# Kernel optimization log

Measured on AMD Instinct MI355X. Metric: run time of the kernel, lower is better.

## Reference

```python
import jax, jax.numpy as jnp
import numpy as np

B, N, H = 128, 512, 512
NEG_INF = -1e30


def setup_inputs() -> dict:
    key = jax.random.key(0)
    k1, k2, k3, k4 = jax.random.split(key, 4)
    code_feat = jax.random.normal(k1, (B, N, H), dtype=jnp.float32)
    node_mask = jax.random.randint(k2, (B, N), 0, 2, dtype=jnp.int32)
    node_mask = node_mask.at[:, 0].set(1)  # ensure >=1 valid node per sample
    scale = 1.0 / np.sqrt(H)
    W_sa = jax.random.normal(k3, (H, H), dtype=jnp.float32) * scale
    b_sa = jnp.zeros((H,), dtype=jnp.float32)
    w_sc = jax.random.normal(k4, (H,), dtype=jnp.float32) * scale
    b_sc = jnp.zeros((), dtype=jnp.float32)
    return {"code_feat": code_feat, "node_mask": node_mask,
            "W_sa": W_sa, "b_sa": b_sa, "w_sc": w_sc, "b_sc": b_sc}


def reference(code_feat, node_mask, W_sa, b_sa, w_sc, b_sc):
    # code_sa_tanh = self_atten_scalar(tanh(self_atten(code_feat)))  -> [B, N]
    h = jnp.tanh(jnp.einsum('bnh,hk->bnk', code_feat, W_sa) + b_sa)
    scores = jnp.einsum('bnk,k->bn', h, w_sc) + b_sc  # [B, N]
    valid = node_mask.astype(bool)
    # masked_select + softmax over selected nodes == masked softmax; invalid
    # positions get weight 0, so the weighted sum over all nodes matches the
    # original per-sample bmm over the ragged selection exactly.
    scores = jnp.where(valid, scores, NEG_INF)
    attn = jax.nn.softmax(scores, axis=1)  # [B, N]
    pooled = jnp.einsum('bn,bnh->bh', attn, code_feat)  # [B, H]
    return jnp.tanh(pooled)
```

## Files before the change

### kernel.cpp

```cpp
#include <hip/hip_runtime.h>

#define NEG_INF (-1e30f)

typedef __bf16 bf16x8 __attribute__((ext_vector_type(8)));
typedef float  f32x4  __attribute__((ext_vector_type(4)));
typedef unsigned short ushort;

__device__ __forceinline__ float fast_tanhf(float x) {
    return 1.0f - 2.0f / (1.0f + __expf(2.0f * x));
}

__device__ __forceinline__ ushort f2bf(float f) {
    union { float f; unsigned u; } v; v.f = f;
    unsigned r = v.u + 0x7fffu + ((v.u >> 16) & 1u);
    return (ushort)(r >> 16);
}

__device__ __forceinline__ void gload_lds16(const void* gsrc, void* ldsdst) {
    __builtin_amdgcn_global_load_lds(
        (const __attribute__((address_space(1))) unsigned int*)gsrc,
        (__attribute__((address_space(3))) unsigned int*)ldsdst, 16, 0, 0);
}

__global__ void convw_kernel(const float* __restrict__ W, ushort* __restrict__ Wt) {
    int i = blockIdx.x * 256 + threadIdx.x;
    int h = i >> 9, c = i & 511;
    Wt[c * 512 + h] = f2bf(W[i]);
}

__global__ __launch_bounds__(256) void gemm_scores_kernel(
    const float* __restrict__ feat, const ushort* __restrict__ Wt,
    const float* __restrict__ b_sa, const float* __restrict__ w_sc,
    float* __restrict__ sp) {

    __shared__ ushort Alds[2][4096];
    __shared__ ushort Blds[2][4096];
    __shared__ float  redE[4][64];

    const int tid  = threadIdx.x;
    const int id   = blockIdx.x;
    const int g    = id & 7;
    const int c8   = id >> 3;
    const int my   = g * 64 + (c8 >> 2);
    const int by   = c8 & 3;
    const int m0   = my * 128;
    const int n0   = by * 128;

    const int lane = tid & 63;
    const int wv   = tid >> 6;
    const int wm   = wv >> 1, wn = wv & 1;
    const int lr   = lane & 15;
    const int kg   = lane >> 4;

    const int arow = tid >> 1;
    const int aseg = (tid & 1) * 16;
    const float* agp = feat + (size_t)(m0 + arow) * 512 + aseg;
    const int wA = (arow >> 4) * 512 + (aseg >> 3) * 128 + (arow & 15) * 8;

    const ushort* bg0 = Wt + (size_t)(n0 + (0 * 4 + wv) * 16 + lr) * 512 + kg * 8;
    const ushort* bg1 = Wt + (size_t)(n0 + (1 * 4 + wv) * 16 + lr) * 512 + kg * 8;

    const int aBase = wm * 2048 + kg * 128 + lr * 8;
    const int bBase = wn * 2048 + kg * 128 + lr * 8;

    f32x4 acc[4][4];
#pragma unroll
    for (int a = 0; a < 4; ++a)
#pragma unroll
        for (int b = 0; b < 4; ++b) acc[a][b] = (f32x4){0.f, 0.f, 0.f, 0.f};

    float4 p0 = *reinterpret_cast<const float4*>(agp + 0);
    float4 p1 = *reinterpret_cast<const float4*>(agp + 4);
    float4 p2 = *reinterpret_cast<const float4*>(agp + 8);
    float4 p3 = *reinterpret_cast<const float4*>(agp + 12);
    gload_lds16(bg0, (char*)Blds[0] + wv * 1024);
    gload_lds16(bg1, (char*)Blds[0] + 4096 + wv * 1024);
    {
        bf16x8 h0, h1;
        h0[0] = (__bf16)p0.x; h0[1] = (__bf16)p0.y; h0[2] = (__bf16)p0.z; h0[3] = (__bf16)p0.w;
        h0[4] = (__bf16)p1.x; h0[5] = (__bf16)p1.y; h0[6] = (__bf16)p1.z; h0[7] = (__bf16)p1.w;
        h1[0] = (__bf16)p2.x; h1[1] = (__bf16)p2.y; h1[2] = (__bf16)p2.z; h1[3] = (__bf16)p2.w;
        h1[4] = (__bf16)p3.x; h1[5] = (__bf16)p3.y; h1[6] = (__bf16)p3.z; h1[7] = (__bf16)p3.w;
        *reinterpret_cast<bf16x8*>(&Alds[0][wA])       = h0;
        *reinterpret_cast<bf16x8*>(&Alds[0][wA + 128]) = h1;
    }
    p0 = *reinterpret_cast<const float4*>(agp + 32);
    p1 = *reinterpret_cast<const float4*>(agp + 36);
    p2 = *reinterpret_cast<const float4*>(agp + 40);
    p3 = *reinterpret_cast<const float4*>(agp + 44);
    __syncthreads();

    int p = 0;
    for (int k0 = 0; k0 < 512; k0 += 32) {
        if (k0 < 480) {
            bf16x8 h0, h1;
            h0[0] = (__bf16)p0.x; h0[1] = (__bf16)p0.y; h0[2] = (__bf16)p0.z; h0[3] = (__bf16)p0.w;
            h0[4] = (__bf16)p1.x; h0[5] = (__bf16)p1.y; h0[6] = (__bf16)p1.z; h0[7] = (__bf16)p1.w;
            h1[0] = (__bf16)p2.x; h1[1] = (__bf16)p2.y; h1[2] = (__bf16)p2.z; h1[3] = (__bf16)p2.w;
            h1[4] = (__bf16)p3.x; h1[5] = (__bf16)p3.y; h1[6] = (__bf16)p3.z; h1[7] = (__bf16)p3.w;
            *reinterpret_cast<bf16x8*>(&Alds[p ^ 1][wA])       = h0;
            *reinterpret_cast<bf16x8*>(&Alds[p ^ 1][wA + 128]) = h1;
            gload_lds16(bg0 + k0 + 32, (char*)Blds[p ^ 1] + wv * 1024);
            gload_lds16(bg1 + k0 + 32, (char*)Blds[p ^ 1] + 4096 + wv * 1024);
            if (k0 < 448) {
                p0 = *reinterpret_cast<const float4*>(agp + k0 + 64);
                p1 = *reinterpret_cast<const float4*>(agp + k0 + 68);
                p2 = *reinterpret_cast<const float4*>(agp + k0 + 72);
                p3 = *reinterpret_cast<const float4*>(agp + k0 + 76);
            }
        }
        bf16x8 af[4], bfv[4];
#pragma unroll
        for (int a = 0; a < 4; ++a)
            af[a] = *reinterpret_cast<const bf16x8*>(&Alds[p][aBase + a * 512]);
#pragma unroll
        for (int b = 0; b < 4; ++b)
            bfv[b] = *reinterpret_cast<const bf16x8*>(&Blds[p][bBase + b * 512]);
#pragma unroll
        for (int a = 0; a < 4; ++a)
#pragma unroll
            for (int b = 0; b < 4; ++b)
                acc[a][b] = __builtin_amdgcn_mfma_f32_16x16x32_bf16(
                    af[a], bfv[b], acc[a][b], 0, 0, 0);
        __syncthreads();
        p ^= 1;
    }

    float rsum[4][4];
#pragma unroll
    for (int a = 0; a < 4; ++a)
#pragma unroll
        for (int r = 0; r < 4; ++r) rsum[a][r] = 0.0f;

#pragma unroll
    for (int b = 0; b < 4; ++b) {
        int col = n0 + wn * 64 + b * 16 + lr;
        float wsc = w_sc[col];
        float bsa = b_sa[col];
#pragma unroll
        for (int a = 0; a < 4; ++a)
#pragma unroll
            for (int r = 0; r < 4; ++r)
                rsum[a][r] += fast_tanhf(acc[a][b][r] + bsa) * wsc;
    }
#pragma unroll
    for (int a = 0; a < 4; ++a)
#pragma unroll
        for (int r = 0; r < 4; ++r) {
            float v = rsum[a][r];
            v += __shfl_xor(v, 1);
            v += __shfl_xor(v, 2);
            v += __shfl_xor(v, 4);
            v += __shfl_xor(v, 8);
            rsum[a][r] = v;
        }
    if (lr == 0) {
#pragma unroll
        for (int a = 0; a < 4; ++a)
#pragma unroll
            for (int r = 0; r < 4; ++r)
                redE[wv][a * 16 + kg * 4 + r] = rsum[a][r];
    }
    __syncthreads();
    if (tid < 128) {
        int wmo = tid >> 6, r64 = tid & 63;
        sp[(size_t)by * 65536 + m0 + tid] = redE[wmo * 2][r64] + redE[wmo * 2 + 1][r64];
    }
}

__global__ void softmax_kernel(const float* __restrict__ sp, const float* __restrict__ b_sc,
                               const int* __restrict__ mask, float* __restrict__ probs) {
    int b = blockIdx.x, t = threadIdx.x;
    int i0 = b * 512 + t, i1 = i0 + 256;
    float s0 = sp[i0] + sp[65536 + i0] + sp[131072 + i0] + sp[196608 + i0] + b_sc[0];
    float s1 = sp[i1] + sp[65536 + i1] + sp[131072 + i1] + sp[196608 + i1] + b_sc[0];
    if (!mask[i0]) s0 = NEG_INF;
    if (!mask[i1]) s1 = NEG_INF;
    float m = fmaxf(s0, s1);
#pragma unroll
    for (int o = 1; o < 64; o <<= 1) m = fmaxf(m, __shfl_xor(m, o));
    __shared__ float red[4];
    if ((t & 63) == 0) red[t >> 6] = m;
    __syncthreads();
    m = fmaxf(fmaxf(red[0], red[1]), fmaxf(red[2], red[3]));
    float e0 = __expf(s0 - m), e1 = __expf(s1 - m);
    float z = e0 + e1;
#pragma unroll
    for (int o = 1; o < 64; o <<= 1) z += __shfl_xor(z, o);
    __syncthreads();
    if ((t & 63) == 0) red[t >> 6] = z;
    __syncthreads();
    float inv = 1.0f / (red[0] + red[1] + red[2] + red[3]);
    probs[i0] = e0 * inv;
    probs[i1] = e1 * inv;
}

__global__ void pool_kernel(const float* __restrict__ feat,
                            const float* __restrict__ probs,
                            float* __restrict__ part) {
    int b = blockIdx.x, c = blockIdx.y, t = threadIdx.x;
    __shared__ float pl[128];
    __shared__ float red2[2][512];
    if (t < 128) pl[t] = probs[b * 512 + c * 128 + t];
    __syncthreads();
    int col4 = (t & 127) * 4;
    int stripe = t >> 7;
    const float* fb = feat + ((size_t)(b * 512 + c * 128 + stripe * 64)) * 512 + col4;
    float4 a4 = {0.f, 0.f, 0.f, 0.f};
#pragma unroll 8
    for (int n = 0; n < 64; ++n) {
        float p = pl[stripe * 64 + n];
        const float4 f4 = *reinterpret_cast<const float4*>(fb + (size_t)n * 512);
        a4.x = fmaf(p, f4.x, a4.x);
        a4.y = fmaf(p, f4.y, a4.y);
        a4.z = fmaf(p, f4.z, a4.z);
        a4.w = fmaf(p, f4.w, a4.w);
    }
    *reinterpret_cast<float4*>(&red2[stripe][col4]) = a4;
    __syncthreads();
    float x0 = red2[0][t] + red2[1][t];
    float x1 = red2[0][t + 256] + red2[1][t + 256];
    part[(size_t)c * 65536 + b * 512 + t]       = x0;
    part[(size_t)c * 65536 + b * 512 + t + 256] = x1;
}

__global__ void finish_kernel(const float* __restrict__ part, float* __restrict__ out) {
    int i = blockIdx.x * 256 + threadIdx.x;
    float s = part[i] + part[65536 + i] + part[131072 + i] + part[196608 + i];
    out[i] = fast_tanhf(s);
}

extern "C" void kernel_launch(void* const* d_in, const int* in_sizes, int n_in,
                              void* d_out, int out_size, void* d_ws, size_t ws_size,
                              hipStream_t stream) {
    const float* feat = (const float*)d_in[0];
    const int*   mask = (const int*)d_in[1];
    const float* W_sa = (const float*)d_in[2];
    const float* b_sa = (const float*)d_in[3];
    const float* w_sc = (const float*)d_in[4];
    const float* b_sc = (const float*)d_in[5];
    float* out = (float*)d_out;

    char* ws = (char*)d_ws;
    ushort* Wt    = (ushort*)ws;
    float*  sp    = (float*)(ws + (512 << 10));
    float*  probs = (float*)(ws + (512 << 10) + (1024 << 10));
    float*  part  = (float*)(ws + (512 << 10) + (1280 << 10));

    hipLaunchKernelGGL(convw_kernel, dim3(1024), dim3(256), 0, stream, W_sa, Wt);
    hipLaunchKernelGGL(gemm_scores_kernel, dim3(2048), dim3(256), 0, stream,
                       feat, Wt, b_sa, w_sc, sp);
    hipLaunchKernelGGL(softmax_kernel, dim3(128), dim3(256), 0, stream,
                       sp, b_sc, mask, probs);
    hipLaunchKernelGGL(pool_kernel, dim3(128, 4), dim3(256), 0, stream, feat, probs, part);
    hipLaunchKernelGGL(finish_kernel, dim3(256), dim3(256), 0, stream, part, out);
}
```

Baseline: 107.4 us.

## Replace LDS double buffering with single buffer and raise occupancy hint

Drops the double-buffered A/B tiles in shared memory for a single buffer. Each k-step now loads B, writes A, synchronizes, prefetches the next A slice into registers, computes, and synchronizes again. It adds a minimum-blocks hint of 5 to launch_bounds and uses the hardware reciprocal in tanh. The aim is to cut LDS use and registers so more blocks fit per CU, trading away the overlap between loads and MFMA within each block.

```diff
diff --git a/kernel.cpp b/kernel.cpp
--- a/kernel.cpp
+++ b/kernel.cpp
@@ -7,7 +7,8 @@
 typedef unsigned short ushort;
 
 __device__ __forceinline__ float fast_tanhf(float x) {
-    return 1.0f - 2.0f / (1.0f + __expf(2.0f * x));
+    float e = __expf(2.0f * x);
+    return 1.0f - 2.0f * __builtin_amdgcn_rcpf(1.0f + e);
 }
 
 __device__ __forceinline__ ushort f2bf(float f) {
@@ -28,13 +29,13 @@
     Wt[c * 512 + h] = f2bf(W[i]);
 }
 
-__global__ __launch_bounds__(256) void gemm_scores_kernel(
+__global__ __launch_bounds__(256, 5) void gemm_scores_kernel(
     const float* __restrict__ feat, const ushort* __restrict__ Wt,
     const float* __restrict__ b_sa, const float* __restrict__ w_sc,
     float* __restrict__ sp) {
 
-    __shared__ ushort Alds[2][4096];
-    __shared__ ushort Blds[2][4096];
+    __shared__ ushort Alds[4096];
+    __shared__ ushort Blds[4096];
     __shared__ float  redE[4][64];
 
     const int tid  = threadIdx.x;
@@ -73,49 +74,35 @@
     float4 p1 = *reinterpret_cast<const float4*>(agp + 4);
     float4 p2 = *reinterpret_cast<const float4*>(agp + 8);
     float4 p3 = *reinterpret_cast<const float4*>(agp + 12);
-    gload_lds16(bg0, (char*)Blds[0] + wv * 1024);
-    gload_lds16(bg1, (char*)Blds[0] + 4096 + wv * 1024);
-    {
-        bf16x8 h0, h1;
-        h0[0] = (__bf16)p0.x; h0[1] = (__bf16)p0.y; h0[2] = (__bf16)p0.z; h0[3] = (__bf16)p0.w;
-        h0[4] = (__bf16)p1.x; h0[5] = (__bf16)p1.y; h0[6] = (__bf16)p1.z; h0[7] = (__bf16)p1.w;
-        h1[0] = (__bf16)p2.x; h1[1] = (__bf16)p2.y; h1[2] = (__bf16)p2.z; h1[3] = (__bf16)p2.w;
-        h1[4] = (__bf16)p3.x; h1[5] = (__bf16)p3.y; h1[6] = (__bf16)p3.z; h1[7] = (__bf16)p3.w;
-        *reinterpret_cast<bf16x8*>(&Alds[0][wA])       = h0;
-        *reinterpret_cast<bf16x8*>(&Alds[0][wA + 128]) = h1;
-    }
-    p0 = *reinterpret_cast<const float4*>(agp + 32);
-    p1 = *reinterpret_cast<const float4*>(agp + 36);
-    p2 = *reinterpret_cast<const float4*>(agp + 40);
-    p3 = *reinterpret_cast<const float4*>(agp + 44);
-    __syncthreads();
-
-    int p = 0;
+
     for (int k0 = 0; k0 < 512; k0 += 32) {
-        if (k0 < 480) {
+        gload_lds16(bg0 + k0, (char*)Blds + wv * 1024);
+        gload_lds16(bg1 + k0, (char*)Blds + 4096 + wv * 1024);
+        {
             bf16x8 h0, h1;
             h0[0] = (__bf16)p0.x; h0[1] = (__bf16)p0.y; h0[2] = (__bf16)p0.z; h0[3] = (__bf16)p0.w;
             h0[4] = (__bf16)p1.x; h0[5] = (__bf16)p1.y; h0[6] = (__bf16)p1.z; h0[7] = (__bf16)p1.w;
             h1[0] = (__bf16)p2.x; h1[1] = (__bf16)p2.y; h1[2] = (__bf16)p2.z; h1[3] = (__bf16)p2.w;
             h1[4] = (__bf16)p3.x; h1[5] = (__bf16)p3.y; h1[6] = (__bf16)p3.z; h1[7] = (__bf16)p3.w;
-            *reinterpret_cast<bf16x8*>(&Alds[p ^ 1][wA])       = h0;
-            *reinterpret_cast<bf16x8*>(&Alds[p ^ 1][wA + 128]) = h1;
-            gload_lds16(bg0 + k0 + 32, (char*)Blds[p ^ 1] + wv * 1024);
-            gload_lds16(bg1 + k0 + 32, (char*)Blds[p ^ 1] + 4096 + wv * 1024);
-            if (k0 < 448) {
-                p0 = *reinterpret_cast<const float4*>(agp + k0 + 64);
-                p1 = *reinterpret_cast<const float4*>(agp + k0 + 68);
-                p2 = *reinterpret_cast<const float4*>(agp + k0 + 72);
-                p3 = *reinterpret_cast<const float4*>(agp + k0 + 76);
-            }
+            *reinterpret_cast<bf16x8*>(&Alds[wA])       = h0;
+            *reinterpret_cast<bf16x8*>(&Alds[wA + 128]) = h1;
         }
+        __syncthreads();
+
+        if (k0 < 480) {
+            p0 = *reinterpret_cast<const float4*>(agp + k0 + 32);
+            p1 = *reinterpret_cast<const float4*>(agp + k0 + 36);
+            p2 = *reinterpret_cast<const float4*>(agp + k0 + 40);
+            p3 = *reinterpret_cast<const float4*>(agp + k0 + 44);
+        }
+
         bf16x8 af[4], bfv[4];
 #pragma unroll
         for (int a = 0; a < 4; ++a)
-            af[a] = *reinterpret_cast<const bf16x8*>(&Alds[p][aBase + a * 512]);
+            af[a] = *reinterpret_cast<const bf16x8*>(&Alds[aBase + a * 512]);
 #pragma unroll
         for (int b = 0; b < 4; ++b)
-            bfv[b] = *reinterpret_cast<const bf16x8*>(&Blds[p][bBase + b * 512]);
+            bfv[b] = *reinterpret_cast<const bf16x8*>(&Blds[bBase + b * 512]);
 #pragma unroll
         for (int a = 0; a < 4; ++a)
 #pragma unroll
@@ -123,7 +110,6 @@
                 acc[a][b] = __builtin_amdgcn_mfma_f32_16x16x32_bf16(
                     af[a], bfv[b], acc[a][b], 0, 0, 0);
         __syncthreads();
-        p ^= 1;
     }
 
     float rsum[4][4];
```

Result: slower. 173.5 us (+61.6%).
